# Performance work log

Hardware: AMD Instinct MI355X
Metric: run time of the kernel (lower is better)

Reference implementation:

```python
import jax, jax.numpy as jnp
import numpy as np

D_MODEL = 1024
N_HEADS = 16
D_K = D_MODEL // N_HEADS  # 64
D_FF = 2688
THETA = 10000.0
EPS = 1e-5
B, S = 2, 2048


def _rmsnorm(x, w):
    xf = x.astype(jnp.float32)
    ms = jnp.mean(xf * xf, axis=-1, keepdims=True)
    return (xf * w * jax.lax.rsqrt(ms + EPS)).astype(x.dtype)


def _rope(x, cos, sin):
    # x: [B, S, H, D_K]; cos/sin: [S, D_K//2]
    xe = x[..., 0::2]
    xo = x[..., 1::2]
    c = cos[None, :, None, :]
    s = sin[None, :, None, :]
    re = xe * c - xo * s
    ro = xe * s + xo * c
    # interleave back to even/odd layout
    return jnp.stack([re, ro], axis=-1).reshape(x.shape)


def setup_inputs() -> dict:
    key = jax.random.key(0)
    ks = jax.random.split(key, 12)
    sc = 0.02  # keep activations numerically sane (stand-in for trunc_normal init)
    return {
        "x": jax.random.normal(ks[0], (B, S, D_MODEL), dtype=jnp.float32),
        "ln1_w": jax.random.normal(ks[1], (D_MODEL,), dtype=jnp.float32) * sc + 1.0,
        "q_w": jax.random.normal(ks[2], (D_MODEL, D_MODEL), dtype=jnp.float32) * sc,
        "k_w": jax.random.normal(ks[3], (D_MODEL, D_MODEL), dtype=jnp.float32) * sc,
        "v_w": jax.random.normal(ks[4], (D_MODEL, D_MODEL), dtype=jnp.float32) * sc,
        "o_w": jax.random.normal(ks[5], (D_MODEL, D_MODEL), dtype=jnp.float32) * sc,
        "ln2_w": jax.random.normal(ks[6], (D_MODEL,), dtype=jnp.float32) * sc + 1.0,
        "w1_w": jax.random.normal(ks[7], (D_FF, D_MODEL), dtype=jnp.float32) * sc,
        "w3_w": jax.random.normal(ks[8], (D_FF, D_MODEL), dtype=jnp.float32) * sc,
        "w2_w": jax.random.normal(ks[9], (D_MODEL, D_FF), dtype=jnp.float32) * sc,
        "token_positions": jnp.arange(S, dtype=jnp.int32),
    }


def reference(x, ln1_w, q_w, k_w, v_w, o_w, ln2_w, w1_w, w3_w, w2_w, token_positions):
    b, s, _ = x.shape
    # --- pre-norm attention sublayer ---
    h = _rmsnorm(x, ln1_w)
    Q = (h @ q_w.T).reshape(b, s, N_HEADS, D_K)
    K = (h @ k_w.T).reshape(b, s, N_HEADS, D_K)
    V = (h @ v_w.T).reshape(b, s, N_HEADS, D_K)

    # RoPE tables from token positions
    pos = token_positions.astype(jnp.float32)                      # [S]
    kk = jnp.arange(D_K // 2, dtype=jnp.float32)
    inv_freq = THETA ** (-2.0 * kk / D_K)                          # [D_K/2]
    ang = pos[:, None] * inv_freq[None, :]                          # [S, D_K/2]
    cos, sin = jnp.cos(ang), jnp.sin(ang)

    Qr = _rope(Q, cos, sin)
    Kr = _rope(K, cos, sin)

    scale = 1.0 / jnp.sqrt(jnp.float32(D_K))
    scores = jnp.einsum("bqhd,bkhd->bhqk", Qr, Kr) * scale          # [B,H,S,S]
    causal = jnp.tril(jnp.ones((s, s), dtype=bool))
    scores = jnp.where(causal[None, None], scores, jnp.float32(-10000.0))
    attn = jax.nn.softmax(scores, axis=-1)
    ctx = jnp.einsum("bhqk,bkhd->bqhd", attn, V).reshape(b, s, D_MODEL)
    x1 = x + ctx @ o_w.T

    # --- pre-norm SwiGLU FFN sublayer ---
    h2 = _rmsnorm(x1, ln2_w)
    g = h2 @ w1_w.T                                                 # [B,S,D_FF]
    u = h2 @ w3_w.T
    ffn = (g * jax.nn.sigmoid(g) * u) @ w2_w.T
    return x1 + ffn
```

## Files before the change

kernel.cpp:

```cpp
#include <hip/hip_runtime.h>
#include <cstdint>

#define DM   1024
#define NH   16
#define DK   64
#define DFF  2688
#define SEQ  2048
#define BB   2
#define MTOT (BB*SEQ)

typedef __attribute__((ext_vector_type(8))) short short8;
typedef __attribute__((ext_vector_type(4))) float f32x4;

typedef const __attribute__((address_space(1))) void* gaddr_t;
typedef __attribute__((address_space(3))) void* laddr_t;
#define GLOAD_LDS16(g, l) __builtin_amdgcn_global_load_lds((gaddr_t)(g), (laddr_t)(l), 16, 0, 0)
#define MFMA16(a, b, c) __builtin_amdgcn_mfma_f32_16x16x32_bf16((a), (b), (c), 0, 0, 0)
#define WAIT_LDS() __builtin_amdgcn_s_waitcnt(0xc07f)

__device__ __forceinline__ float bf2f(unsigned short u) {
    union { unsigned int i; float f; } v; v.i = ((unsigned int)u) << 16; return v.f;
}
__device__ __forceinline__ unsigned short f2bf(float f) {
    union { float f; unsigned int i; } v; v.f = f;
    unsigned int r = v.i + 0x7fffu + ((v.i >> 16) & 1u);
    return (unsigned short)(r >> 16);
}
__device__ __forceinline__ unsigned long long pack4bf(float a, float b, float c, float d) {
    return (unsigned long long)f2bf(a) | ((unsigned long long)f2bf(b) << 16)
         | ((unsigned long long)f2bf(c) << 32) | ((unsigned long long)f2bf(d) << 48);
}

__global__ __launch_bounds__(256)
void prep_k(const float* __restrict__ q_w, const float* __restrict__ k_w,
            const float* __restrict__ v_w, const float* __restrict__ o_w,
            const float* __restrict__ w1_w, const float* __restrict__ w3_w,
            const float* __restrict__ w2_w,
            unsigned short* __restrict__ Wqkv, unsigned short* __restrict__ Wo,
            unsigned short* __restrict__ W13, unsigned short* __restrict__ W2) {
    const int blk = blockIdx.x;
    const float* src; unsigned short* dst; int cols, rmul, roff, i;
    if (blk < 4096) {
        const int rr = blk >> 10;
        i = (blk & 1023) * 256 + threadIdx.x;
        cols = 1024; rmul = 1;
        if (rr == 0)      { src = q_w; dst = Wqkv; roff = 0; }
        else if (rr == 1) { src = k_w; dst = Wqkv; roff = 1024; }
        else if (rr == 2) { src = v_w; dst = Wqkv; roff = 2048; }
        else              { src = o_w; dst = Wo;   roff = 0; }
    } else if (blk < 6784) {
        i = (blk - 4096) * 256 + threadIdx.x; src = w1_w; dst = W13; cols = 1024; rmul = 2; roff = 0;
    } else if (blk < 9472) {
        i = (blk - 6784) * 256 + threadIdx.x; src = w3_w; dst = W13; cols = 1024; rmul = 2; roff = 1;
    } else {
        i = (blk - 9472) * 256 + threadIdx.x; src = w2_w; dst = W2;  cols = 2688; rmul = 1; roff = 0;
    }
    const int e = i * 4;
    const int r = e / cols, c = e - r * cols;
    const float4 v = *(const float4*)(src + e);
    ushort4 o;
    o.x = f2bf(v.x); o.y = f2bf(v.y); o.z = f2bf(v.z); o.w = f2bf(v.w);
    *(ushort4*)(dst + (size_t)(r * rmul + roff) * cols + c) = o;
}

__global__ __launch_bounds__(256)
void rmsnorm_k(const float* __restrict__ x, const float* __restrict__ w,
               unsigned short* __restrict__ out) {
    const int row = blockIdx.x;
    const int tid = threadIdx.x;
    const float4 v = ((const float4*)(x + (size_t)row * DM))[tid];
    float ss = v.x * v.x + v.y * v.y + v.z * v.z + v.w * v.w;
#pragma unroll
    for (int off = 32; off > 0; off >>= 1) ss += __shfl_down(ss, off, 64);
    __shared__ float sred[4];
    const int wave = tid >> 6, lane = tid & 63;
    if (lane == 0) sred[wave] = ss;
    __syncthreads();
    const float tot = sred[0] + sred[1] + sred[2] + sred[3];
    const float rinv = rsqrtf(tot * (1.0f / DM) + 1e-5f);
    const float4 wv = ((const float4*)w)[tid];
    ushort4 o;
    o.x = f2bf(v.x * wv.x * rinv);
    o.y = f2bf(v.y * wv.y * rinv);
    o.z = f2bf(v.z * wv.z * rinv);
    o.w = f2bf(v.w * wv.w * rinv);
    ((ushort4*)(out + (size_t)row * DM))[tid] = o;
}

__global__ void rope_tab_k(const int* __restrict__ pos, float* __restrict__ tab) {
    const int s = blockIdx.x, t = threadIdx.x;
    const int kk = t & 31;
    const float ang = (float)pos[s] * __expf(-0.28782313662f * (float)kk);
    tab[s * 64 + t] = (t < 32) ? cosf(ang) : sinf(ang);
}

template <int EPI>
__global__ __launch_bounds__(512, 2)
void gemm_big(const unsigned short* __restrict__ A,
              const unsigned short* __restrict__ B,
              unsigned short* __restrict__ O0,
              unsigned short* __restrict__ O1,
              unsigned short* __restrict__ O2,
              const float* __restrict__ ROPT,
              int N, int K) {
    __shared__ unsigned short As[8192];
    __shared__ unsigned short Bs[16384];
    const int tid = threadIdx.x;
    const int wave = tid >> 6, lane = tid & 63;
    const int l15 = lane & 15, quad = lane >> 4;
    const int m0 = blockIdx.y * 128, n0 = blockIdx.x * 256;
    const int wr = (wave >> 2) * 64, wc = (wave & 3) * 64;

    const f32x4 z4 = {0.f, 0.f, 0.f, 0.f};
    f32x4 acc[4][4];
#pragma unroll
    for (int i = 0; i < 4; i++)
#pragma unroll
        for (int j = 0; j < 4; j++) acc[i][j] = z4;

    const unsigned short* pa[2];
    const unsigned short* pb[4];
    int la[2], lb[4];
#pragma unroll
    for (int r = 0; r < 2; r++) {
        const int s = r * 512 + tid;
        pa[r] = A + (size_t)(m0 + (s & 127)) * K + (s >> 7) * 8;
        la[r] = (r * 512 + wave * 64) * 8;
    }
#pragma unroll
    for (int r = 0; r < 4; r++) {
        const int s = r * 512 + tid;
        pb[r] = B + (size_t)(n0 + (s & 255)) * K + (s >> 8) * 8;
        lb[r] = (r * 512 + wave * 64) * 8;
    }

    for (int k0 = 0; k0 < K; k0 += 64) {
        __syncthreads();
#pragma unroll
        for (int r = 0; r < 2; r++) { GLOAD_LDS16(pa[r], &As[la[r]]); pa[r] += 64; }
#pragma unroll
        for (int r = 0; r < 4; r++) { GLOAD_LDS16(pb[r], &Bs[lb[r]]); pb[r] += 64; }
        __syncthreads();
#pragma unroll
        for (int kk = 0; kk < 2; kk++) {
            short8 af[4], bg[4];
#pragma unroll
            for (int t = 0; t < 4; t++)
                af[t] = *(const short8*)(&As[((quad + 4 * kk) * 128 + wr + t * 16 + l15) * 8]);
#pragma unroll
            for (int t = 0; t < 4; t++)
                bg[t] = *(const short8*)(&Bs[((quad + 4 * kk) * 256 + wc + t * 16 + l15) * 8]);
#pragma unroll
            for (int i = 0; i < 4; i++)
#pragma unroll
                for (int j = 0; j < 4; j++)
                    acc[i][j] = MFMA16(bg[j], af[i], acc[i][j]);
        }
    }

#pragma unroll
    for (int i = 0; i < 4; i++) {
        const int r = m0 + wr + i * 16 + l15;
        if (EPI == 0) {
            const int b = r >> 11, s = r & (SEQ - 1);
            const float* rt = ROPT + s * 64;
#pragma unroll
            for (int j = 0; j < 4; j++) {
                const int cb = n0 + wc + j * 16;
                const int sec = cb >> 10;
                const int h = (cb & 1023) >> 6;
                const int cc0 = (cb & 63) + quad * 4;
                const f32x4 a = acc[i][j];
                if (sec < 2) {
                    const int p0 = cc0 >> 1;
                    const float cA = rt[p0],     sA = rt[32 + p0];
                    const float cB = rt[p0 + 1], sB = rt[32 + p0 + 1];
                    const float e0 = a[0] * cA - a[1] * sA;
                    const float o0 = a[0] * sA + a[1] * cA;
                    const float e1 = a[2] * cB - a[3] * sB;
                    const float o1 = a[2] * sB + a[3] * cB;
                    unsigned short* dst = (sec == 0) ? O0 : O1;
                    *(unsigned long long*)(dst + ((size_t)(b * NH + h) * SEQ + s) * DK + cc0) =
                        pack4bf(e0, o0, e1, o1);
                } else {
                    unsigned short* dst = O2 + ((size_t)(b * NH + h) * DK) * SEQ + s;
#pragma unroll
                    for (int t = 0; t < 4; t++)
                        dst[(size_t)(cc0 + t) * SEQ] = f2bf(a[t]);
                }
            }
        } else {
#pragma unroll
            for (int j = 0; j < 4; j++) {
                const int cc = n0 + wc + j * 16 + quad * 4;
                const f32x4 a = acc[i][j];
                const float s1 = a[0] * a[1] / (1.f + __expf(-a[0]));
                const float s2 = a[2] * a[3] / (1.f + __expf(-a[2]));
                *(unsigned int*)(O0 + (size_t)r * (DFF) + (cc >> 1)) =
                    (unsigned int)f2bf(s1) | ((unsigned int)f2bf(s2) << 16);
            }
        }
    }
}

__global__ __launch_bounds__(256, 4)
void gemm_thin(const unsigned short* __restrict__ A,
               const unsigned short* __restrict__ B,
               float* __restrict__ Cf,
               const float* __restrict__ R,
               int N, int K) {
    __shared__ unsigned short As[8192];
    __shared__ unsigned short Bs[4096];
    const int tid = threadIdx.x;
    const int wave = tid >> 6, lane = tid & 63;
    const int l15 = lane & 15, quad = lane >> 4;
    const int m0 = blockIdx.y * 128, n0 = blockIdx.x * 64;
    const int wr = (wave & 1) * 64, wc = (wave >> 1) * 32;

    const f32x4 z4 = {0.f, 0.f, 0.f, 0.f};
    f32x4 acc[4][2];
#pragma unroll
    for (int i = 0; i < 4; i++)
#pragma unroll
        for (int j = 0; j < 2; j++) acc[i][j] = z4;

    const unsigned short* ap[4];
    int al[4];
#pragma unroll
    for (int i = 0; i < 4; i++) {
        const int s = i * 256 + tid;
        ap[i] = A + (size_t)(m0 + (s & 127)) * K + (s >> 7) * 8;
        al[i] = (i * 256 + wave * 64) * 8;
    }
    const unsigned short* bp[2];
    int bl[2];
#pragma unroll
    for (int i = 0; i < 2; i++) {
        const int s = i * 256 + tid;
        bp[i] = B + (size_t)(n0 + (s & 63)) * K + (s >> 6) * 8;
        bl[i] = (i * 256 + wave * 64) * 8;
    }

    const int nk = K >> 6;
    for (int kc = 0; kc < nk; kc++) {
        __syncthreads();
#pragma unroll
        for (int i = 0; i < 4; i++) { GLOAD_LDS16(ap[i], &As[al[i]]); ap[i] += 64; }
#pragma unroll
        for (int i = 0; i < 2; i++) { GLOAD_LDS16(bp[i], &Bs[bl[i]]); bp[i] += 64; }
        __syncthreads();
#pragma unroll
        for (int h = 0; h < 2; h++) {
            short8 af[4], bg[2];
#pragma unroll
            for (int t = 0; t < 4; t++)
                af[t] = *(const short8*)(&As[((quad + 4 * h) * 128 + wr + t * 16 + l15) * 8]);
#pragma unroll
            for (int t = 0; t < 2; t++)
                bg[t] = *(const short8*)(&Bs[((quad + 4 * h) * 64 + wc + t * 16 + l15) * 8]);
#pragma unroll
            for (int i = 0; i < 4; i++)
#pragma unroll
                for (int j = 0; j < 2; j++)
                    acc[i][j] = MFMA16(bg[j], af[i], acc[i][j]);
        }
    }

#pragma unroll
    for (int i = 0; i < 4; i++) {
        const int r = m0 + wr + i * 16 + l15;
#pragma unroll
        for (int j = 0; j < 2; j++) {
            const int cc = n0 + wc + j * 16 + quad * 4;
            const size_t idx = (size_t)r * N + cc;
            const float4 rv = *(const float4*)(R + idx);
            float4 ov;
            ov.x = acc[i][j][0] + rv.x;
            ov.y = acc[i][j][1] + rv.y;
            ov.z = acc[i][j][2] + rv.z;
            ov.w = acc[i][j][3] + rv.w;
            *(float4*)(Cf + idx) = ov;
        }
    }
}

template <bool MASK>
__device__ __forceinline__ void softmax_tile(f32x4 st[4], float& li, unsigned short* Pw,
                                             int l15, int quad, int j0, int myq) {
    float lsum = 0.f;
#pragma unroll
    for (int t = 0; t < 4; t++) {
#pragma unroll
        for (int r = 0; r < 4; r++) {
            float v = st[t][r] * 0.125f;
            if (MASK) {
                const int key = j0 + t * 16 + quad * 4 + r;
                if (key > myq) v = -1e30f;
            }
            const float p = __expf(v);
            st[t][r] = p;
            lsum += p;
        }
        *(unsigned long long*)(Pw + l15 * 72 + t * 16 + quad * 4) =
            pack4bf(st[t][0], st[t][1], st[t][2], st[t][3]);
    }
    li += lsum;
}

__global__ __launch_bounds__(256, 2)
void attn_k(const unsigned short* __restrict__ Qr, const unsigned short* __restrict__ Kr,
            const unsigned short* __restrict__ Vt, unsigned short* __restrict__ ctx) {
    __shared__ unsigned short KVl[2][8192];
    __shared__ unsigned short Pl[4 * 2 * 1152];
    const int tid = threadIdx.x;
    const int wave = tid >> 6, lane = tid & 63;
    const int l15 = lane & 15, quad = lane >> 4;
    const int bh = blockIdx.y, b = bh >> 4, h = bh & 15;
    const int g = blockIdx.x;
    const int qtA = g * 4 + wave, qtB = 127 - qtA;
    const int q0A = qtA * 16, q0B = qtB * 16;
    const int countA = g + 1, countB = 32 - g;
    const unsigned short* Kb = Kr + (size_t)bh * SEQ * DK;
    const unsigned short* Vb = Vt + (size_t)bh * DK * SEQ;

    const unsigned short* QbA = Qr + ((size_t)bh * SEQ + q0A) * DK;
    const unsigned short* QbB = Qr + ((size_t)bh * SEQ + q0B) * DK;
    const short8 qfA0 = *(const short8*)(QbA + l15 * DK + quad * 8);
    const short8 qfA1 = *(const short8*)(QbA + l15 * DK + 32 + quad * 8);
    const short8 qfB0 = *(const short8*)(QbB + l15 * DK + quad * 8);
    const short8 qfB1 = *(const short8*)(QbB + l15 * DK + 32 + quad * 8);

    const int slot0 = wave * 128 + lane, slot1 = slot0 + 64;
    const int ck0 = slot0 >> 3, s0 = slot0 & 7;
    const int ck1 = slot1 >> 3, s1 = slot1 & 7;
    const unsigned short* kp0 = Kb + ck0 * 64 + (s0 ^ (ck0 & 7)) * 8;
    const unsigned short* kp1 = Kb + ck1 * 64 + (s1 ^ (ck1 & 7)) * 8;
    const unsigned short* vp0 = Vb + ck0 * 2048 + (s0 ^ (ck0 & 7)) * 8;
    const unsigned short* vp1 = Vb + ck1 * 2048 + (s1 ^ (ck1 & 7)) * 8;
    const int kb0 = wave * 1024, kb1 = kb0 + 512;

    unsigned short* PA = Pl + (wave * 2 + 0) * 1152;
    unsigned short* PB = Pl + (wave * 2 + 1) * 1152;

    const f32x4 z4 = {0.f, 0.f, 0.f, 0.f};
    f32x4 oA[4], oB[4];
#pragma unroll
    for (int d = 0; d < 4; d++) { oA[d] = z4; oB[d] = z4; }
    float liA = 0.f, liB = 0.f;
    const int myqA = q0A + l15, myqB = q0B + l15;
    const int xr = l15 & 7;

    GLOAD_LDS16(kp0, &KVl[0][kb0]);
    GLOAD_LDS16(kp1, &KVl[0][kb1]);
    GLOAD_LDS16(vp0, &KVl[0][4096 + kb0]);
    GLOAD_LDS16(vp1, &KVl[0][4096 + kb1]);
    kp0 += 4096; kp1 += 4096; vp0 += 64; vp1 += 64;

    for (int j = 0; j < countB; ++j) {
        const int bf = j & 1;
        const unsigned short* Kl = KVl[bf];
        const unsigned short* Vl = KVl[bf] + 4096;
        __syncthreads();
        if (j + 1 < countB) {
            GLOAD_LDS16(kp0, &KVl[bf ^ 1][kb0]);
            GLOAD_LDS16(kp1, &KVl[bf ^ 1][kb1]);
            GLOAD_LDS16(vp0, &KVl[bf ^ 1][4096 + kb0]);
            GLOAD_LDS16(vp1, &KVl[bf ^ 1][4096 + kb1]);
            kp0 += 4096; kp1 += 4096; vp0 += 64; vp1 += 64;
        }
        const int j0 = j * 64;
        short8 kf[4][2];
#pragma unroll
        for (int t = 0; t < 4; t++) {
            const unsigned short* kr = Kl + (t * 16 + l15) * 64;
            kf[t][0] = *(const short8*)(kr + (quad ^ xr) * 8);
            kf[t][1] = *(const short8*)(kr + ((4 + quad) ^ xr) * 8);
        }
        f32x4 stB[4];
#pragma unroll
        for (int t = 0; t < 4; t++)
            stB[t] = MFMA16(kf[t][1], qfB1, MFMA16(kf[t][0], qfB0, z4));
        const bool doA = (j < countA);
        if (doA) {
            f32x4 stA[4];
#pragma unroll
            for (int t = 0; t < 4; t++)
                stA[t] = MFMA16(kf[t][1], qfA1, MFMA16(kf[t][0], qfA0, z4));
            if (j == countA - 1) softmax_tile<true >(stA, liA, PA, l15, quad, j0, myqA);
            else                 softmax_tile<false>(stA, liA, PA, l15, quad, j0, myqA);
        }
        if (j == countB - 1) softmax_tile<true >(stB, liB, PB, l15, quad, j0, myqB);
        else                 softmax_tile<false>(stB, liB, PB, l15, quad, j0, myqB);
        WAIT_LDS();
        short8 vf[4][2];
#pragma unroll
        for (int dt = 0; dt < 4; dt++) {
            const unsigned short* vr = Vl + (dt * 16 + l15) * 64;
            vf[dt][0] = *(const short8*)(vr + (quad ^ xr) * 8);
            vf[dt][1] = *(const short8*)(vr + ((4 + quad) ^ xr) * 8);
        }
        {
            const short8 pfB0 = *(const short8*)(PB + l15 * 72 + quad * 8);
            const short8 pfB1 = *(const short8*)(PB + l15 * 72 + 32 + quad * 8);
#pragma unroll
            for (int dt = 0; dt < 4; dt++)
                oB[dt] = MFMA16(vf[dt][1], pfB1, MFMA16(vf[dt][0], pfB0, oB[dt]));
        }
        if (doA) {
            const short8 pfA0 = *(const short8*)(PA + l15 * 72 + quad * 8);
            const short8 pfA1 = *(const short8*)(PA + l15 * 72 + 32 + quad * 8);
#pragma unroll
            for (int dt = 0; dt < 4; dt++)
                oA[dt] = MFMA16(vf[dt][1], pfA1, MFMA16(vf[dt][0], pfA0, oA[dt]));
        }
    }
    liA += __shfl_xor(liA, 16, 64); liA += __shfl_xor(liA, 32, 64);
    liB += __shfl_xor(liB, 16, 64); liB += __shfl_xor(liB, 32, 64);
    const float invA = 1.0f / liA, invB = 1.0f / liB;
#pragma unroll
    for (int dt = 0; dt < 4; dt++) {
        *(unsigned long long*)(PA + l15 * 72 + dt * 16 + quad * 4) =
            pack4bf(oA[dt][0] * invA, oA[dt][1] * invA, oA[dt][2] * invA, oA[dt][3] * invA);
        *(unsigned long long*)(PB + l15 * 72 + dt * 16 + quad * 4) =
            pack4bf(oB[dt][0] * invB, oB[dt][1] * invB, oB[dt][2] * invB, oB[dt][3] * invB);
    }
    WAIT_LDS();
    const int row = lane >> 2, seg = (lane & 3) * 8;
#pragma unroll
    for (int p = 0; p < 2; p++) {
        const int cs = seg + p * 32;
        const uint4 va = *(const uint4*)(PA + row * 72 + cs);
        *(uint4*)(ctx + ((size_t)b * SEQ + q0A + row) * DM + h * DK + cs) = va;
        const uint4 vb = *(const uint4*)(PB + row * 72 + cs);
        *(uint4*)(ctx + ((size_t)b * SEQ + q0B + row) * DM + h * DK + cs) = vb;
    }
}

extern "C" void kernel_launch(void* const* d_in, const int* in_sizes, int n_in,
                              void* d_out, int out_size, void* d_ws, size_t ws_size,
                              hipStream_t stream) {
    const float* x     = (const float*)d_in[0];
    const float* ln1_w = (const float*)d_in[1];
    const float* q_w   = (const float*)d_in[2];
    const float* k_w   = (const float*)d_in[3];
    const float* v_w   = (const float*)d_in[4];
    const float* o_w   = (const float*)d_in[5];
    const float* ln2_w = (const float*)d_in[6];
    const float* w1_w  = (const float*)d_in[7];
    const float* w3_w  = (const float*)d_in[8];
    const float* w2_w  = (const float*)d_in[9];
    const int*   tpos  = (const int*)d_in[10];
    float* out = (float*)d_out;
    char* ws = (char*)d_ws;

    unsigned short* Wqkv = (unsigned short*)(ws + 0);
    unsigned short* Wo   = (unsigned short*)(ws + 6291456);
    unsigned short* W13  = (unsigned short*)(ws + 8388608);
    unsigned short* W2   = (unsigned short*)(ws + 19398656);
    float*          X1   = (float*)(ws + 24903680);
    float*          ROPT = (float*)(ws + 24903680);
    char* base = ws + 41680896;
    unsigned short* H    = (unsigned short*)(base);
    unsigned short* QR   = (unsigned short*)(base + 8388608);
    unsigned short* KR   = (unsigned short*)(base + 16777216);
    unsigned short* VT   = (unsigned short*)(base + 25165824);
    unsigned short* CTX  = (unsigned short*)(base + 33554432);
    unsigned short* H2   = (unsigned short*)(base);
    unsigned short* ACT  = (unsigned short*)(base + 41943040);

    prep_k<<<12160, 256, 0, stream>>>(q_w, k_w, v_w, o_w, w1_w, w3_w, w2_w,
                                      Wqkv, Wo, W13, W2);
    rope_tab_k<<<2048, 64, 0, stream>>>(tpos, ROPT);

    rmsnorm_k<<<4096, 256, 0, stream>>>(x, ln1_w, H);
    gemm_big<0><<<dim3(12, 32), 512, 0, stream>>>(H, Wqkv, QR, KR, VT, ROPT, 3072, 1024);
    attn_k<<<dim3(16, 32), 256, 0, stream>>>(QR, KR, VT, CTX);
    gemm_thin<<<dim3(16, 32), 256, 0, stream>>>(CTX, Wo, X1, x, 1024, 1024);
    rmsnorm_k<<<4096, 256, 0, stream>>>(X1, ln2_w, H2);
    gemm_big<1><<<dim3(21, 32), 512, 0, stream>>>(H2, W13, ACT, nullptr, nullptr, nullptr, 5376, 1024);
    gemm_thin<<<dim3(16, 32), 256, 0, stream>>>(ACT, W2, out, X1, 1024, 2688);
}
```

Measured before the change: 449.4 us.

## Double-buffer gemm_big LDS loads, switch to 256x128 tiles with XCD-aware block swizzle

gemm_big now double-buffers its A/B LDS tiles so the global-to-LDS loads for the next K step are issued before the MFMAs on the current one, with explicit vmcnt waits and barriers in place of two __syncthreads per iteration. The block tile changes from 128x256 to 256x128 with a 4x2 wave arrangement, the launch grids are adjusted to match, and block indices are remapped in groups of eight for L2/XCD locality. s_setprio is raised around the MFMA section. LDS use doubles to 96KB per block and the occupancy hint of 2 blocks per CU is dropped, so fewer blocks may be resident at once. The epilogue still depends on the new wr/wc/m0/n0 mapping being correct.

```diff
diff --git a/kernel.cpp b/kernel.cpp
--- a/kernel.cpp
+++ b/kernel.cpp
@@ -17,6 +17,11 @@
 #define GLOAD_LDS16(g, l) __builtin_amdgcn_global_load_lds((gaddr_t)(g), (laddr_t)(l), 16, 0, 0)
 #define MFMA16(a, b, c) __builtin_amdgcn_mfma_f32_16x16x32_bf16((a), (b), (c), 0, 0, 0)
 #define WAIT_LDS() __builtin_amdgcn_s_waitcnt(0xc07f)
+
+#define VMCNT(n) asm volatile("s_waitcnt vmcnt(" #n ")" ::: "memory")
+#define BAR() do { asm volatile("" ::: "memory"); \
+                   __builtin_amdgcn_s_barrier();  \
+                   asm volatile("" ::: "memory"); } while (0)
 
 __device__ __forceinline__ float bf2f(unsigned short u) {
     union { unsigned int i; float f; } v; v.i = ((unsigned int)u) << 16; return v.f;
@@ -95,7 +100,7 @@
 }
 
 template <int EPI>
-__global__ __launch_bounds__(512, 2)
+__global__ __launch_bounds__(512)
 void gemm_big(const unsigned short* __restrict__ A,
               const unsigned short* __restrict__ B,
               unsigned short* __restrict__ O0,
@@ -103,13 +108,20 @@
               unsigned short* __restrict__ O2,
               const float* __restrict__ ROPT,
               int N, int K) {
-    __shared__ unsigned short As[8192];
-    __shared__ unsigned short Bs[16384];
+    __shared__ unsigned short As[2][16384];
+    __shared__ unsigned short Bs[2][8192];
     const int tid = threadIdx.x;
     const int wave = tid >> 6, lane = tid & 63;
     const int l15 = lane & 15, quad = lane >> 4;
-    const int m0 = blockIdx.y * 128, n0 = blockIdx.x * 256;
-    const int wr = (wave >> 2) * 64, wc = (wave & 3) * 64;
+
+    const int gx = gridDim.x;
+    const int nwg = gx * gridDim.y;
+    const int lin = blockIdx.y * gx + blockIdx.x;
+    const int swz = (lin & 7) * (nwg >> 3) + (lin >> 3);
+    const int bx = swz % gx, by = swz / gx;
+
+    const int m0 = by * 256, n0 = bx * 128;
+    const int wr = (wave >> 1) * 64, wc = (wave & 1) * 64;
 
     const f32x4 z4 = {0.f, 0.f, 0.f, 0.f};
     f32x4 acc[4][4];
@@ -118,44 +130,63 @@
 #pragma unroll
         for (int j = 0; j < 4; j++) acc[i][j] = z4;
 
-    const unsigned short* pa[2];
-    const unsigned short* pb[4];
-    int la[2], lb[4];
+    const unsigned short* pa[4];
+    const unsigned short* pb[2];
+    int la[4], lb[2];
+#pragma unroll
+    for (int r = 0; r < 4; r++) {
+        const int s = r * 512 + tid;
+        pa[r] = A + (size_t)(m0 + (s & 255)) * K + (s >> 8) * 8;
+        la[r] = (r * 512 + wave * 64) * 8;
+    }
 #pragma unroll
     for (int r = 0; r < 2; r++) {
         const int s = r * 512 + tid;
-        pa[r] = A + (size_t)(m0 + (s & 127)) * K + (s >> 7) * 8;
-        la[r] = (r * 512 + wave * 64) * 8;
-    }
-#pragma unroll
-    for (int r = 0; r < 4; r++) {
-        const int s = r * 512 + tid;
-        pb[r] = B + (size_t)(n0 + (s & 255)) * K + (s >> 8) * 8;
+        pb[r] = B + (size_t)(n0 + (s & 127)) * K + (s >> 7) * 8;
         lb[r] = (r * 512 + wave * 64) * 8;
     }
 
-    for (int k0 = 0; k0 < K; k0 += 64) {
-        __syncthreads();
-#pragma unroll
-        for (int r = 0; r < 2; r++) { GLOAD_LDS16(pa[r], &As[la[r]]); pa[r] += 64; }
-#pragma unroll
-        for (int r = 0; r < 4; r++) { GLOAD_LDS16(pb[r], &Bs[lb[r]]); pb[r] += 64; }
-        __syncthreads();
+    const int nt = K >> 6;
+
+#pragma unroll
+    for (int r = 0; r < 4; r++) { GLOAD_LDS16(pa[r], &As[0][la[r]]); pa[r] += 64; }
+#pragma unroll
+    for (int r = 0; r < 2; r++) { GLOAD_LDS16(pb[r], &Bs[0][lb[r]]); pb[r] += 64; }
+    VMCNT(0);
+    BAR();
+
+    int cur = 0;
+    for (int t = 0; t < nt; ++t) {
+        if (t + 1 < nt) {
+            const int nb = cur ^ 1;
+#pragma unroll
+            for (int r = 0; r < 4; r++) { GLOAD_LDS16(pa[r], &As[nb][la[r]]); pa[r] += 64; }
+#pragma unroll
+            for (int r = 0; r < 2; r++) { GLOAD_LDS16(pb[r], &Bs[nb][lb[r]]); pb[r] += 64; }
+            VMCNT(6);
+        } else {
+            VMCNT(0);
+        }
+        BAR();
+        __builtin_amdgcn_s_setprio(1);
 #pragma unroll
         for (int kk = 0; kk < 2; kk++) {
             short8 af[4], bg[4];
 #pragma unroll
-            for (int t = 0; t < 4; t++)
-                af[t] = *(const short8*)(&As[((quad + 4 * kk) * 128 + wr + t * 16 + l15) * 8]);
-#pragma unroll
-            for (int t = 0; t < 4; t++)
-                bg[t] = *(const short8*)(&Bs[((quad + 4 * kk) * 256 + wc + t * 16 + l15) * 8]);
+            for (int tt = 0; tt < 4; tt++)
+                af[tt] = *(const short8*)(&As[cur][((quad + 4 * kk) * 256 + wr + tt * 16 + l15) * 8]);
+#pragma unroll
+            for (int tt = 0; tt < 4; tt++)
+                bg[tt] = *(const short8*)(&Bs[cur][((quad + 4 * kk) * 128 + wc + tt * 16 + l15) * 8]);
 #pragma unroll
             for (int i = 0; i < 4; i++)
 #pragma unroll
                 for (int j = 0; j < 4; j++)
                     acc[i][j] = MFMA16(bg[j], af[i], acc[i][j]);
         }
+        __builtin_amdgcn_s_setprio(0);
+        BAR();
+        cur ^= 1;
     }
 
 #pragma unroll
@@ -473,10 +504,10 @@
     rope_tab_k<<<2048, 64, 0, stream>>>(tpos, ROPT);
 
     rmsnorm_k<<<4096, 256, 0, stream>>>(x, ln1_w, H);
-    gemm_big<0><<<dim3(12, 32), 512, 0, stream>>>(H, Wqkv, QR, KR, VT, ROPT, 3072, 1024);
+    gemm_big<0><<<dim3(24, 16), 512, 0, stream>>>(H, Wqkv, QR, KR, VT, ROPT, 3072, 1024);
     attn_k<<<dim3(16, 32), 256, 0, stream>>>(QR, KR, VT, CTX);
     gemm_thin<<<dim3(16, 32), 256, 0, stream>>>(CTX, Wo, X1, x, 1024, 1024);
     rmsnorm_k<<<4096, 256, 0, stream>>>(X1, ln2_w, H2);
-    gemm_big<1><<<dim3(21, 32), 512, 0, stream>>>(H2, W13, ACT, nullptr, nullptr, nullptr, 5376, 1024);
+    gemm_big<1><<<dim3(42, 16), 512, 0, stream>>>(H2, W13, ACT, nullptr, nullptr, nullptr, 5376, 1024);
     gemm_thin<<<dim3(16, 32), 256, 0, stream>>>(ACT, W2, out, X1, 1024, 2688);
 }
```

After: 480.1 us. 1.07x slower.
